# Optimization experiments

Measured on AMD Instinct MI355X. Metric: run time of the kernel, lower is better.

The kernel has to match this reference:

```python
import jax, jax.numpy as jnp
import numpy as np

DIM_Q = 1024
DIM_K = 1024
DIM_V = 1024


def setup_inputs() -> dict:
    key = jax.random.key(0)
    kx, kq, kk, kv = jax.random.split(key, 4)
    x = jax.random.normal(kx, (4, 2048, DIM_Q), dtype=jnp.float32)
    # torch nn.Linear weights: [out_features, in_features], y = x @ W.T
    scale = 1.0 / np.sqrt(DIM_Q)
    Wq = jax.random.uniform(kq, (DIM_K, DIM_Q), dtype=jnp.float32, minval=-scale, maxval=scale)
    Wk = jax.random.uniform(kk, (DIM_K, DIM_Q), dtype=jnp.float32, minval=-scale, maxval=scale)
    Wv = jax.random.uniform(kv, (DIM_V, DIM_Q), dtype=jnp.float32, minval=-scale, maxval=scale)
    return {"x": x, "Wq": Wq, "Wk": Wk, "Wv": Wv}


def reference(x, Wq, Wk, Wv):
    # q, k: [b, s, dim_k]; v: [b, s, dim_v]
    q = jnp.einsum('bsd,kd->bsk', x, Wq)
    k = jnp.einsum('bsd,kd->bsk', x, Wk)
    v = jnp.einsum('bsd,vd->bsv', x, Wv)
    norm_fact = 1.0 / jnp.sqrt(jnp.asarray(DIM_K, dtype=x.dtype))
    score = jnp.einsum('bik,bjk->bij', q, k) * norm_fact  # [b, s, s]
    score = jax.nn.softmax(score, axis=-1)
    att = jnp.einsum('bij,bjv->biv', score, v)
    att = att + v  # is_residual=True
    return att
```

## Files before the change

kernel.cpp:

```cpp
#include <hip/hip_runtime.h>
#include <hip/hip_bf16.h>

using bf16 = __hip_bfloat16;
typedef __attribute__((ext_vector_type(8))) short short8;
typedef __attribute__((ext_vector_type(4))) float floatx4;
typedef __attribute__((ext_vector_type(8))) int int8v;

__device__ __forceinline__ void async_ld16(const void* g, void* l) {
  __builtin_amdgcn_global_load_lds((const __attribute__((address_space(1))) void*)g,
                                   (__attribute__((address_space(3))) void*)l, 16, 0, 0);
}

__device__ __forceinline__ int pk4_fp8(float a, float b, float c, float d) {
  int v = __builtin_amdgcn_cvt_pk_fp8_f32(a, b, 0, false);
  return __builtin_amdgcn_cvt_pk_fp8_f32(c, d, v, true);
}


__device__ __forceinline__ void gemm_core(const bf16* __restrict__ At,
                                          const bf16* __restrict__ Bt,
                                          int K, bf16* lA, bf16* lB,
                                          floatx4 acc[4][4]) {
  const int tid  = threadIdx.x;
  const int w    = tid >> 6;
  const int lane = tid & 63;
  const int subM = (w >> 1) * 64;
  const int subN = (w & 1) * 64;
  const int fr   = lane & 15;
  const int fq   = lane >> 4;

  int srow[4], scol[4], sdst[4];
#pragma unroll
  for (int q = 0; q < 4; ++q) {
    int p = q * 256 + w * 64 + lane;
    int r = p >> 3;
    int j = (p & 7) ^ (r & 7);
    srow[q] = r;
    scol[q] = j * 8;
    sdst[q] = (q * 256 + w * 64) * 8;
  }
  int offA[2][4], offB[2][4];
#pragma unroll
  for (int kc = 0; kc < 2; ++kc)
#pragma unroll
    for (int i = 0; i < 4; ++i) {
      int rA = subM + i * 16 + fr;
      offA[kc][i] = (rA * 8 + ((kc * 4 + fq) ^ (rA & 7))) * 8;
      int rB = subN + i * 16 + fr;
      offB[kc][i] = (rB * 8 + ((kc * 4 + fq) ^ (rB & 7))) * 8;
    }

  floatx4 zero = {0.f, 0.f, 0.f, 0.f};
#pragma unroll
  for (int i = 0; i < 4; ++i)
#pragma unroll
    for (int j = 0; j < 4; ++j) acc[i][j] = zero;

  for (int k0 = 0; k0 < K; k0 += 64) {
    __syncthreads();
#pragma unroll
    for (int q = 0; q < 4; ++q) {
      async_ld16(At + (size_t)srow[q] * K + k0 + scol[q], lA + sdst[q]);
      async_ld16(Bt + (size_t)srow[q] * K + k0 + scol[q], lB + sdst[q]);
    }
    __syncthreads();
#pragma unroll
    for (int kc = 0; kc < 2; ++kc) {
      short8 a[4], b[4];
#pragma unroll
      for (int i = 0; i < 4; ++i) a[i] = *(const short8*)(lA + offA[kc][i]);
#pragma unroll
      for (int j = 0; j < 4; ++j) b[j] = *(const short8*)(lB + offB[kc][j]);
#pragma unroll
      for (int i = 0; i < 4; ++i)
#pragma unroll
        for (int j = 0; j < 4; ++j)
          acc[i][j] = __builtin_amdgcn_mfma_f32_16x16x32_bf16(a[i], b[j], acc[i][j], 0, 0, 0);
    }
  }
}

__device__ __forceinline__ void gemm_core_f8(const unsigned char* __restrict__ At,
                                             const unsigned char* __restrict__ Bt,
                                             int K, unsigned char* lA, unsigned char* lB,
                                             floatx4 acc[4][4]) {
  const int tid  = threadIdx.x;
  const int w    = tid >> 6;
  const int lane = tid & 63;
  const int subM = (w >> 1) * 64;
  const int subN = (w & 1) * 64;
  const int fr   = lane & 15;
  const int fq   = lane >> 4;

  int srow[4], scol[4], sdst[4];
#pragma unroll
  for (int q = 0; q < 4; ++q) {
    int p = q * 256 + w * 64 + lane;
    int r = p >> 3;
    int j = (p & 7) ^ (r & 7);
    srow[q] = r;
    scol[q] = j * 16;
    sdst[q] = (q * 256 + w * 64) * 16;
  }
  int offA[2][4], offB[2][4];
#pragma unroll
  for (int h = 0; h < 2; ++h)
#pragma unroll
    for (int i = 0; i < 4; ++i) {
      int rA = subM + i * 16 + fr;
      offA[h][i] = rA * 128 + (((fq * 2 + h) ^ (rA & 7)) * 16);
      int rB = subN + i * 16 + fr;
      offB[h][i] = rB * 128 + (((fq * 2 + h) ^ (rB & 7)) * 16);
    }

  floatx4 zero = {0.f, 0.f, 0.f, 0.f};
#pragma unroll
  for (int i = 0; i < 4; ++i)
#pragma unroll
    for (int j = 0; j < 4; ++j) acc[i][j] = zero;

  for (int k0 = 0; k0 < K; k0 += 128) {
    __syncthreads();
#pragma unroll
    for (int q = 0; q < 4; ++q) {
      async_ld16(At + (size_t)srow[q] * K + k0 + scol[q], lA + sdst[q]);
      async_ld16(Bt + (size_t)srow[q] * K + k0 + scol[q], lB + sdst[q]);
    }
    __syncthreads();
    int8v a[4], b[4];
#pragma unroll
    for (int i = 0; i < 4; ++i) {
      int4 lo = *(const int4*)(lA + offA[0][i]);
      int4 hi = *(const int4*)(lA + offA[1][i]);
      int8v v;
      v[0] = lo.x; v[1] = lo.y; v[2] = lo.z; v[3] = lo.w;
      v[4] = hi.x; v[5] = hi.y; v[6] = hi.z; v[7] = hi.w;
      a[i] = v;
    }
#pragma unroll
    for (int j = 0; j < 4; ++j) {
      int4 lo = *(const int4*)(lB + offB[0][j]);
      int4 hi = *(const int4*)(lB + offB[1][j]);
      int8v v;
      v[0] = lo.x; v[1] = lo.y; v[2] = lo.z; v[3] = lo.w;
      v[4] = hi.x; v[5] = hi.y; v[6] = hi.z; v[7] = hi.w;
      b[j] = v;
    }
#pragma unroll
    for (int i = 0; i < 4; ++i)
#pragma unroll
      for (int j = 0; j < 4; ++j)
        acc[i][j] = __builtin_amdgcn_mfma_scale_f32_16x16x128_f8f6f4(
            a[i], b[j], acc[i][j], 0, 0, 0, 0x7F7F7F7F, 0, 0x7F7F7F7F);
  }
}

__global__ __launch_bounds__(256) void proj_gemm(
    const bf16* __restrict__ Xbf, const bf16* __restrict__ Wvbf, bf16* __restrict__ Vbf,
    const unsigned char* __restrict__ X8, const unsigned char* __restrict__ Wq8,
    const unsigned char* __restrict__ Wk8,
    unsigned char* __restrict__ Qf8, unsigned char* __restrict__ Kf8) {
  __shared__ __align__(16) char lds[32768];
  const int id = blockIdx.x;
  const int tid = threadIdx.x, w = tid >> 6, lane = tid & 63;
  const int subM = (w >> 1) * 64, subN = (w & 1) * 64;
  const int fr = lane & 15, fq = lane >> 4;

  if (id < 512) {
    const int r = id & 7, g = id >> 3;
    const int ty = r * 8 + (g & 7), tx = g >> 3;
    bf16* lA = (bf16*)lds;
    bf16* lB = (bf16*)(lds + 16384);
    floatx4 acc[4][4];
    gemm_core(Xbf + (size_t)ty * 128 * 1024, Wvbf + (size_t)tx * 128 * 1024,
              1024, lA, lB, acc);
    const int rowBase = ty * 128 + subM;
    const int colBase = tx * 128 + subN;
#pragma unroll
    for (int i = 0; i < 4; ++i)
#pragma unroll
      for (int j = 0; j < 4; ++j)
#pragma unroll
        for (int rr = 0; rr < 4; ++rr) {
          int row = rowBase + i * 16 + fq * 4 + rr;
          int col = colBase + j * 16 + fr;
          Vbf[(size_t)row * 1024 + col] = __float2bfloat16(acc[i][j][rr]);
        }
  } else {
    const int local = id - 512;
    const int z = local >> 9, lid = local & 511;
    const int r = lid & 7, g = lid >> 3;
    const int ty = r * 8 + (g & 7), tx = g >> 3;
    unsigned char* lA = (unsigned char*)lds;
    unsigned char* lB = (unsigned char*)(lds + 16384);
    floatx4 acc[4][4];
    gemm_core_f8(X8 + (size_t)ty * 128 * 1024,
                 (z == 0 ? Wq8 : Wk8) + (size_t)tx * 128 * 1024, 1024, lA, lB, acc);
    unsigned char* dst = (z == 0) ? Qf8 : Kf8;
    const int rowBase = ty * 128 + subM;
    const int colBase = tx * 128 + subN;
#pragma unroll
    for (int i = 0; i < 4; ++i)
#pragma unroll
      for (int rr = 0; rr < 4; ++rr) {
        int row = rowBase + i * 16 + fq * 4 + rr;
        unsigned int p = (unsigned int)pk4_fp8(acc[i][0][rr], acc[i][1][rr],
                                               acc[i][2][rr], acc[i][3][rr]);
        *(unsigned int*)&dst[(size_t)row * 1024 + colBase + fr * 4] = p;
      }
  }
}

__global__ __launch_bounds__(256) void mid_kernel(
    const unsigned char* __restrict__ Qf8, const unsigned char* __restrict__ Kf8,
    unsigned char* __restrict__ S8, float* __restrict__ l,
    const bf16* __restrict__ Vbf, unsigned char* __restrict__ Vt8) {
  __shared__ __align__(16) char lds[32768];
  const int id = blockIdx.x;
  const int t = threadIdx.x;

  if (id < 1024) {
    const int r = id & 7, g = id >> 3;
    const int b = g >> 5;
    const int rem = g & 31;
    const int ty = r * 2 + (rem & 1);
    const int tx = rem >> 1;
    unsigned char* lA = (unsigned char*)lds;
    unsigned char* lB = (unsigned char*)(lds + 16384);
    floatx4 acc[4][4];
    gemm_core_f8(Qf8 + (size_t)b * 2048 * 1024 + (size_t)ty * 128 * 1024,
                 Kf8 + (size_t)b * 2048 * 1024 + (size_t)tx * 128 * 1024,
                 1024, lA, lB, acc);
    const int w = t >> 6, lane = t & 63;
    const int subM = (w >> 1) * 64, subN = (w & 1) * 64;
    const int fr = lane & 15, fq = lane >> 4;
    const int rowBase = ty * 128 + subM;
    const int colBase = tx * 128 + subN;
    unsigned char* Sb = S8 + (size_t)b * 2048 * 2048;
    float* lb = l + (size_t)b * 2048;
#pragma unroll
    for (int i = 0; i < 4; ++i)
#pragma unroll
      for (int rr = 0; rr < 4; ++rr) {
        int row = rowBase + i * 16 + fq * 4 + rr;
        unsigned int p = (unsigned int)pk4_fp8(
            __expf(acc[i][0][rr] * 0.03125f), __expf(acc[i][1][rr] * 0.03125f),
            __expf(acc[i][2][rr] * 0.03125f), __expf(acc[i][3][rr] * 0.03125f));
        *(unsigned int*)&Sb[(size_t)row * 2048 + colBase + fr * 4] = p;
        float psum = __builtin_amdgcn_cvt_f32_fp8(p, 0) + __builtin_amdgcn_cvt_f32_fp8(p, 1) +
                     __builtin_amdgcn_cvt_f32_fp8(p, 2) + __builtin_amdgcn_cvt_f32_fp8(p, 3);
        psum += __shfl_xor(psum, 1, 64);
        psum += __shfl_xor(psum, 2, 64);
        psum += __shfl_xor(psum, 4, 64);
        psum += __shfl_xor(psum, 8, 64);
        if (fr == 0) atomicAdd(&lb[row], psum);
      }
  } else {
    const int t2 = id - 1024;
    const int b = t2 >> 9, rem = t2 & 511;
    const int xs = rem & 31, yv = rem >> 5;
    const int s0 = xs * 64, v0 = yv * 64;
    short(*tile)[72] = (short(*)[72])lds;
#pragma unroll
    for (int i = 0; i < 2; ++i) {
      int c = t + i * 256;
      int row = c >> 3, cj = c & 7;
      *(short8*)&tile[row][cj * 8] =
          *(const short8*)&Vbf[((size_t)(b * 2048 + s0 + row)) * 1024 + v0 + cj * 8];
    }
    __syncthreads();
    const int vrow = t >> 2, sq = t & 3;
#pragma unroll
    for (int hc = 0; hc < 2; ++hc) {
      float f[8];
#pragma unroll
      for (int e = 0; e < 8; ++e) {
        int p = sq * 16 + hc * 8 + e;
        int s = (p & 3) * 16 + (p >> 2);
        short sh = tile[s][vrow];
        f[e] = __bfloat162float(*(bf16*)&sh);
      }
      uint2 packed;
      packed.x = (unsigned int)pk4_fp8(f[0], f[1], f[2], f[3]);
      packed.y = (unsigned int)pk4_fp8(f[4], f[5], f[6], f[7]);
      *(uint2*)&Vt8[((size_t)(b * 1024 + v0 + vrow)) * 2048 + s0 + sq * 16 + hc * 8] = packed;
    }
  }
}

__global__ __launch_bounds__(256) void pv_gemm(const unsigned char* __restrict__ S8,
                                               const unsigned char* __restrict__ Vt8,
                                               const bf16* __restrict__ Vbf,
                                               const float* __restrict__ l,
                                               float* __restrict__ out) {
  __shared__ __align__(16) char lds[32768];
  unsigned char* lA = (unsigned char*)lds;
  unsigned char* lB = (unsigned char*)(lds + 16384);
  const int id = blockIdx.x;
  const int r = id & 7, g = id >> 3;
  const int b = g >> 4;
  const int rem = g & 15;
  const int ty = r * 2 + (rem & 1);
  const int tx = rem >> 1;

  floatx4 acc[4][4];
  gemm_core_f8(S8 + (size_t)b * 2048 * 2048 + (size_t)ty * 128 * 2048,
               Vt8 + (size_t)b * 1024 * 2048 + (size_t)tx * 128 * 2048,
               2048, lA, lB, acc);

  const int tid = threadIdx.x, w = tid >> 6, lane = tid & 63;
  const int subM = (w >> 1) * 64, subN = (w & 1) * 64;
  const int fr = lane & 15, fq = lane >> 4;
  const int rowBase = ty * 128 + subM;
  const int colBase = tx * 128 + subN;
  const float* lb = l + (size_t)b * 2048;
#pragma unroll
  for (int i = 0; i < 4; ++i)
#pragma unroll
    for (int rr = 0; rr < 4; ++rr) {
      int row = rowBase + i * 16 + fq * 4 + rr;
      float inv = 1.0f / lb[row];
#pragma unroll
      for (int j = 0; j < 4; ++j) {
        int col = colBase + j * 16 + fr;
        size_t oi = ((size_t)b * 2048 + row) * 1024 + col;
        out[oi] = acc[i][j][rr] * inv + __bfloat162float(Vbf[oi]);
      }
    }
}

__global__ void cast_all(const float* __restrict__ x, const float* __restrict__ wq,
                         const float* __restrict__ wk, const float* __restrict__ wv,
                         bf16* __restrict__ Xbf, unsigned char* __restrict__ X8,
                         unsigned char* __restrict__ Wq8, unsigned char* __restrict__ Wk8,
                         bf16* __restrict__ Wvbf, float* __restrict__ l) {
  const int blk = blockIdx.x;
  const int t = threadIdx.x;
  if (blk < 8192) {
    int i = blk * 256 + t;
    float4 f = ((const float4*)x)[i];
    bf16 tmp[4] = {__float2bfloat16(f.x), __float2bfloat16(f.y),
                   __float2bfloat16(f.z), __float2bfloat16(f.w)};
    ((ushort4*)Xbf)[i] = *(const ushort4*)tmp;
    ((unsigned int*)X8)[i] = (unsigned int)pk4_fp8(f.x, f.y, f.z, f.w);
  } else if (blk < 10240) {
    const float* src = (blk < 9216) ? wq : wk;
    unsigned char* dst = (blk < 9216) ? Wq8 : Wk8;
    int i = ((blk - 8192) & 1023) * 256 + t;
    float4 f = ((const float4*)src)[i];
    ((unsigned int*)dst)[i] = (unsigned int)pk4_fp8(f.x, f.y, f.z, f.w);
  } else if (blk < 11264) {
    int i = (blk - 10240) * 256 + t;
    float4 f = ((const float4*)wv)[i];
    bf16 tmp[4] = {__float2bfloat16(f.x), __float2bfloat16(f.y),
                   __float2bfloat16(f.z), __float2bfloat16(f.w)};
    ((ushort4*)Wvbf)[i] = *(const ushort4*)tmp;
  } else {
    int i = (blk - 11264) * 256 + t;
    ((float4*)l)[i] = make_float4(0.f, 0.f, 0.f, 0.f);
  }
}

extern "C" void kernel_launch(void* const* d_in, const int* in_sizes, int n_in,
                              void* d_out, int out_size, void* d_ws, size_t ws_size,
                              hipStream_t stream) {
  const float* x  = (const float*)d_in[0];
  const float* Wq = (const float*)d_in[1];
  const float* Wk = (const float*)d_in[2];
  const float* Wv = (const float*)d_in[3];
  float* out = (float*)d_out;

  char* ws = (char*)d_ws;
  bf16* Xbf = (bf16*)ws;                   ws += (size_t)8192 * 1024 * 2;
  unsigned char* X8 = (unsigned char*)ws;  ws += (size_t)8192 * 1024;
  unsigned char* Wq8 = (unsigned char*)ws; ws += (size_t)1024 * 1024;
  unsigned char* Wk8 = (unsigned char*)ws; ws += (size_t)1024 * 1024;
  bf16* Wvbf = (bf16*)ws;                  ws += (size_t)1024 * 1024 * 2;
  unsigned char* Qf8 = (unsigned char*)ws; ws += (size_t)8192 * 1024;
  unsigned char* Kf8 = (unsigned char*)ws; ws += (size_t)8192 * 1024;
  bf16* Vbf = (bf16*)ws;                   ws += (size_t)8192 * 1024 * 2;
  unsigned char* Vt8 = (unsigned char*)ws; ws += (size_t)4 * 1024 * 2048;
  unsigned char* S8  = (unsigned char*)ws; ws += (size_t)4 * 2048 * 2048;
  float* l = (float*)ws;                   ws += (size_t)8192 * 4;

  cast_all<<<11272, 256, 0, stream>>>(x, Wq, Wk, Wv, Xbf, X8, Wq8, Wk8, Wvbf, l);
  proj_gemm<<<1536, 256, 0, stream>>>(Xbf, Wvbf, Vbf, X8, Wq8, Wk8, Qf8, Kf8);
  mid_kernel<<<3072, 256, 0, stream>>>(Qf8, Kf8, S8, l, Vbf, Vt8);
  pv_gemm<<<512, 256, 0, stream>>>(S8, Vt8, Vbf, l, out);
}
```

Baseline: 188.1 us.

## Widen FP8 GEMM tiles to 128x256 and extend LDS swizzle

Adds a 128x256 FP8 GEMM core used by the Q/K projection and the QK^T score kernel, which halves the block count and loads each A fragment once for eight MFMA columns instead of four. The LDS XOR swizzle gains an extra bit from row bit 3 to reduce bank conflicts on fragment reads. LDS grows to 48 KB and launch bounds request two blocks per CU. The wider accumulator raises register pressure, and fewer, larger blocks may leave some CUs underused.

```diff
diff --git a/kernel.cpp b/kernel.cpp
--- a/kernel.cpp
+++ b/kernel.cpp
@@ -14,6 +14,14 @@
 __device__ __forceinline__ int pk4_fp8(float a, float b, float c, float d) {
   int v = __builtin_amdgcn_cvt_pk_fp8_f32(a, b, 0, false);
   return __builtin_amdgcn_cvt_pk_fp8_f32(c, d, v, true);
+}
+
+__device__ __forceinline__ int8v ld_frag16(const unsigned char* lo, const unsigned char* hi) {
+  int4 l0 = *(const int4*)lo, h0 = *(const int4*)hi;
+  int8v v;
+  v[0] = l0.x; v[1] = l0.y; v[2] = l0.z; v[3] = l0.w;
+  v[4] = h0.x; v[5] = h0.y; v[6] = h0.z; v[7] = h0.w;
+  return v;
 }
 
 
@@ -97,7 +105,7 @@
   for (int q = 0; q < 4; ++q) {
     int p = q * 256 + w * 64 + lane;
     int r = p >> 3;
-    int j = (p & 7) ^ (r & 7);
+    int j = (p & 7) ^ (r & 7) ^ ((r & 8) >> 1);
     srow[q] = r;
     scol[q] = j * 16;
     sdst[q] = (q * 256 + w * 64) * 16;
@@ -108,9 +116,9 @@
 #pragma unroll
     for (int i = 0; i < 4; ++i) {
       int rA = subM + i * 16 + fr;
-      offA[h][i] = rA * 128 + (((fq * 2 + h) ^ (rA & 7)) * 16);
+      offA[h][i] = rA * 128 + (((fq * 2 + h) ^ (rA & 7) ^ ((rA & 8) >> 1)) * 16);
       int rB = subN + i * 16 + fr;
-      offB[h][i] = rB * 128 + (((fq * 2 + h) ^ (rB & 7)) * 16);
+      offB[h][i] = rB * 128 + (((fq * 2 + h) ^ (rB & 7) ^ ((rB & 8) >> 1)) * 16);
     }
 
   floatx4 zero = {0.f, 0.f, 0.f, 0.f};
@@ -129,23 +137,9 @@
     __syncthreads();
     int8v a[4], b[4];
 #pragma unroll
-    for (int i = 0; i < 4; ++i) {
-      int4 lo = *(const int4*)(lA + offA[0][i]);
-      int4 hi = *(const int4*)(lA + offA[1][i]);
-      int8v v;
-      v[0] = lo.x; v[1] = lo.y; v[2] = lo.z; v[3] = lo.w;
-      v[4] = hi.x; v[5] = hi.y; v[6] = hi.z; v[7] = hi.w;
-      a[i] = v;
-    }
-#pragma unroll
-    for (int j = 0; j < 4; ++j) {
-      int4 lo = *(const int4*)(lB + offB[0][j]);
-      int4 hi = *(const int4*)(lB + offB[1][j]);
-      int8v v;
-      v[0] = lo.x; v[1] = lo.y; v[2] = lo.z; v[3] = lo.w;
-      v[4] = hi.x; v[5] = hi.y; v[6] = hi.z; v[7] = hi.w;
-      b[j] = v;
-    }
+    for (int i = 0; i < 4; ++i) a[i] = ld_frag16(lA + offA[0][i], lA + offA[1][i]);
+#pragma unroll
+    for (int j = 0; j < 4; ++j) b[j] = ld_frag16(lB + offB[0][j], lB + offB[1][j]);
 #pragma unroll
     for (int i = 0; i < 4; ++i)
 #pragma unroll
@@ -155,15 +149,86 @@
   }
 }
 
-__global__ __launch_bounds__(256) void proj_gemm(
+__device__ __forceinline__ void gemm_core_f8_v2(const unsigned char* __restrict__ At,
+                                                const unsigned char* __restrict__ Bt,
+                                                int K, unsigned char* lA, unsigned char* lB,
+                                                floatx4 acc[4][8]) {
+  const int tid  = threadIdx.x;
+  const int w    = tid >> 6;
+  const int lane = tid & 63;
+  const int subM = (w >> 1) * 64;
+  const int subN = (w & 1) * 128;
+  const int fr   = lane & 15;
+  const int fq   = lane >> 4;
+
+  int srowA[4], scolA[4], sdstA[4];
+#pragma unroll
+  for (int q = 0; q < 4; ++q) {
+    int p = q * 256 + w * 64 + lane;
+    int r = p >> 3;
+    int j = (p & 7) ^ (r & 7) ^ ((r & 8) >> 1);
+    srowA[q] = r; scolA[q] = j * 16; sdstA[q] = (q * 256 + w * 64) * 16;
+  }
+  int srowB[8], scolB[8], sdstB[8];
+#pragma unroll
+  for (int q = 0; q < 8; ++q) {
+    int p = q * 256 + w * 64 + lane;
+    int r = p >> 3;
+    int j = (p & 7) ^ (r & 7) ^ ((r & 8) >> 1);
+    srowB[q] = r; scolB[q] = j * 16; sdstB[q] = (q * 256 + w * 64) * 16;
+  }
+  int offA[2][4], offB[2][8];
+#pragma unroll
+  for (int h = 0; h < 2; ++h) {
+#pragma unroll
+    for (int i = 0; i < 4; ++i) {
+      int rA = subM + i * 16 + fr;
+      offA[h][i] = rA * 128 + (((fq * 2 + h) ^ (rA & 7) ^ ((rA & 8) >> 1)) * 16);
+    }
+#pragma unroll
+    for (int j = 0; j < 8; ++j) {
+      int rB = subN + j * 16 + fr;
+      offB[h][j] = rB * 128 + (((fq * 2 + h) ^ (rB & 7) ^ ((rB & 8) >> 1)) * 16);
+    }
+  }
+
+  floatx4 zero = {0.f, 0.f, 0.f, 0.f};
+#pragma unroll
+  for (int i = 0; i < 4; ++i)
+#pragma unroll
+    for (int j = 0; j < 8; ++j) acc[i][j] = zero;
+
+  for (int k0 = 0; k0 < K; k0 += 128) {
+    __syncthreads();
+#pragma unroll
+    for (int q = 0; q < 4; ++q)
+      async_ld16(At + (size_t)srowA[q] * K + k0 + scolA[q], lA + sdstA[q]);
+#pragma unroll
+    for (int q = 0; q < 8; ++q)
+      async_ld16(Bt + (size_t)srowB[q] * K + k0 + scolB[q], lB + sdstB[q]);
+    __syncthreads();
+    int8v a[4];
+#pragma unroll
+    for (int i = 0; i < 4; ++i) a[i] = ld_frag16(lA + offA[0][i], lA + offA[1][i]);
+#pragma unroll
+    for (int j = 0; j < 8; ++j) {
+      int8v bf = ld_frag16(lB + offB[0][j], lB + offB[1][j]);
+#pragma unroll
+      for (int i = 0; i < 4; ++i)
+        acc[i][j] = __builtin_amdgcn_mfma_scale_f32_16x16x128_f8f6f4(
+            a[i], bf, acc[i][j], 0, 0, 0, 0x7F7F7F7F, 0, 0x7F7F7F7F);
+    }
+  }
+}
+
+__global__ __launch_bounds__(256, 2) void proj_gemm(
     const bf16* __restrict__ Xbf, const bf16* __restrict__ Wvbf, bf16* __restrict__ Vbf,
     const unsigned char* __restrict__ X8, const unsigned char* __restrict__ Wq8,
     const unsigned char* __restrict__ Wk8,
     unsigned char* __restrict__ Qf8, unsigned char* __restrict__ Kf8) {
-  __shared__ __align__(16) char lds[32768];
+  __shared__ __align__(16) char lds[49152];
   const int id = blockIdx.x;
   const int tid = threadIdx.x, w = tid >> 6, lane = tid & 63;
-  const int subM = (w >> 1) * 64, subN = (w & 1) * 64;
   const int fr = lane & 15, fq = lane >> 4;
 
   if (id < 512) {
@@ -174,6 +239,7 @@
     floatx4 acc[4][4];
     gemm_core(Xbf + (size_t)ty * 128 * 1024, Wvbf + (size_t)tx * 128 * 1024,
               1024, lA, lB, acc);
+    const int subM = (w >> 1) * 64, subN = (w & 1) * 64;
     const int rowBase = ty * 128 + subM;
     const int colBase = tx * 128 + subN;
 #pragma unroll
@@ -188,54 +254,59 @@
         }
   } else {
     const int local = id - 512;
-    const int z = local >> 9, lid = local & 511;
+    const int z = local >> 8, lid = local & 255;
     const int r = lid & 7, g = lid >> 3;
-    const int ty = r * 8 + (g & 7), tx = g >> 3;
+    const int ty = r * 8 + (g & 7);
+    const int tx = g >> 3;
     unsigned char* lA = (unsigned char*)lds;
     unsigned char* lB = (unsigned char*)(lds + 16384);
-    floatx4 acc[4][4];
-    gemm_core_f8(X8 + (size_t)ty * 128 * 1024,
-                 (z == 0 ? Wq8 : Wk8) + (size_t)tx * 128 * 1024, 1024, lA, lB, acc);
+    floatx4 acc[4][8];
+    gemm_core_f8_v2(X8 + (size_t)ty * 128 * 1024,
+                    (z == 0 ? Wq8 : Wk8) + (size_t)tx * 256 * 1024, 1024, lA, lB, acc);
     unsigned char* dst = (z == 0) ? Qf8 : Kf8;
+    const int subM = (w >> 1) * 64, subN = (w & 1) * 128;
     const int rowBase = ty * 128 + subM;
-    const int colBase = tx * 128 + subN;
+    const int colBase = tx * 256 + subN;
 #pragma unroll
     for (int i = 0; i < 4; ++i)
 #pragma unroll
       for (int rr = 0; rr < 4; ++rr) {
         int row = rowBase + i * 16 + fq * 4 + rr;
-        unsigned int p = (unsigned int)pk4_fp8(acc[i][0][rr], acc[i][1][rr],
-                                               acc[i][2][rr], acc[i][3][rr]);
-        *(unsigned int*)&dst[(size_t)row * 1024 + colBase + fr * 4] = p;
+        unsigned int p0 = (unsigned int)pk4_fp8(acc[i][0][rr], acc[i][1][rr],
+                                                acc[i][2][rr], acc[i][3][rr]);
+        unsigned int p1 = (unsigned int)pk4_fp8(acc[i][4][rr], acc[i][5][rr],
+                                                acc[i][6][rr], acc[i][7][rr]);
+        *(unsigned int*)&dst[(size_t)row * 1024 + colBase + fr * 4] = p0;
+        *(unsigned int*)&dst[(size_t)row * 1024 + colBase + 64 + fr * 4] = p1;
       }
   }
 }
 
-__global__ __launch_bounds__(256) void mid_kernel(
+__global__ __launch_bounds__(256, 2) void mid_kernel(
     const unsigned char* __restrict__ Qf8, const unsigned char* __restrict__ Kf8,
     unsigned char* __restrict__ S8, float* __restrict__ l,
     const bf16* __restrict__ Vbf, unsigned char* __restrict__ Vt8) {
-  __shared__ __align__(16) char lds[32768];
+  __shared__ __align__(16) char lds[49152];
   const int id = blockIdx.x;
   const int t = threadIdx.x;
 
-  if (id < 1024) {
+  if (id < 512) {
     const int r = id & 7, g = id >> 3;
-    const int b = g >> 5;
-    const int rem = g & 31;
+    const int b = g >> 4;
+    const int rem = g & 15;
     const int ty = r * 2 + (rem & 1);
     const int tx = rem >> 1;
     unsigned char* lA = (unsigned char*)lds;
     unsigned char* lB = (unsigned char*)(lds + 16384);
-    floatx4 acc[4][4];
-    gemm_core_f8(Qf8 + (size_t)b * 2048 * 1024 + (size_t)ty * 128 * 1024,
-                 Kf8 + (size_t)b * 2048 * 1024 + (size_t)tx * 128 * 1024,
-                 1024, lA, lB, acc);
+    floatx4 acc[4][8];
+    gemm_core_f8_v2(Qf8 + (size_t)b * 2048 * 1024 + (size_t)ty * 128 * 1024,
+                    Kf8 + (size_t)b * 2048 * 1024 + (size_t)tx * 256 * 1024,
+                    1024, lA, lB, acc);
     const int w = t >> 6, lane = t & 63;
-    const int subM = (w >> 1) * 64, subN = (w & 1) * 64;
+    const int subM = (w >> 1) * 64, subN = (w & 1) * 128;
     const int fr = lane & 15, fq = lane >> 4;
     const int rowBase = ty * 128 + subM;
-    const int colBase = tx * 128 + subN;
+    const int colBase = tx * 256 + subN;
     unsigned char* Sb = S8 + (size_t)b * 2048 * 2048;
     float* lb = l + (size_t)b * 2048;
 #pragma unroll
@@ -243,12 +314,18 @@
 #pragma unroll
       for (int rr = 0; rr < 4; ++rr) {
         int row = rowBase + i * 16 + fq * 4 + rr;
-        unsigned int p = (unsigned int)pk4_fp8(
+        unsigned int p0 = (unsigned int)pk4_fp8(
             __expf(acc[i][0][rr] * 0.03125f), __expf(acc[i][1][rr] * 0.03125f),
             __expf(acc[i][2][rr] * 0.03125f), __expf(acc[i][3][rr] * 0.03125f));
-        *(unsigned int*)&Sb[(size_t)row * 2048 + colBase + fr * 4] = p;
-        float psum = __builtin_amdgcn_cvt_f32_fp8(p, 0) + __builtin_amdgcn_cvt_f32_fp8(p, 1) +
-                     __builtin_amdgcn_cvt_f32_fp8(p, 2) + __builtin_amdgcn_cvt_f32_fp8(p, 3);
+        unsigned int p1 = (unsigned int)pk4_fp8(
+            __expf(acc[i][4][rr] * 0.03125f), __expf(acc[i][5][rr] * 0.03125f),
+            __expf(acc[i][6][rr] * 0.03125f), __expf(acc[i][7][rr] * 0.03125f));
+        *(unsigned int*)&Sb[(size_t)row * 2048 + colBase + fr * 4] = p0;
+        *(unsigned int*)&Sb[(size_t)row * 2048 + colBase + 64 + fr * 4] = p1;
+        float psum = __builtin_amdgcn_cvt_f32_fp8(p0, 0) + __builtin_amdgcn_cvt_f32_fp8(p0, 1) +
+                     __builtin_amdgcn_cvt_f32_fp8(p0, 2) + __builtin_amdgcn_cvt_f32_fp8(p0, 3) +
+                     __builtin_amdgcn_cvt_f32_fp8(p1, 0) + __builtin_amdgcn_cvt_f32_fp8(p1, 1) +
+                     __builtin_amdgcn_cvt_f32_fp8(p1, 2) + __builtin_amdgcn_cvt_f32_fp8(p1, 3);
         psum += __shfl_xor(psum, 1, 64);
         psum += __shfl_xor(psum, 2, 64);
         psum += __shfl_xor(psum, 4, 64);
@@ -256,7 +333,7 @@
         if (fr == 0) atomicAdd(&lb[row], psum);
       }
   } else {
-    const int t2 = id - 1024;
+    const int t2 = id - 512;
     const int b = t2 >> 9, rem = t2 & 511;
     const int xs = rem & 31, yv = rem >> 5;
     const int s0 = xs * 64, v0 = yv * 64;
@@ -384,7 +461,7 @@
   float* l = (float*)ws;                   ws += (size_t)8192 * 4;
 
   cast_all<<<11272, 256, 0, stream>>>(x, Wq, Wk, Wv, Xbf, X8, Wq8, Wk8, Wvbf, l);
-  proj_gemm<<<1536, 256, 0, stream>>>(Xbf, Wvbf, Vbf, X8, Wq8, Wk8, Qf8, Kf8);
-  mid_kernel<<<3072, 256, 0, stream>>>(Qf8, Kf8, S8, l, Vbf, Vt8);
+  proj_gemm<<<1024, 256, 0, stream>>>(Xbf, Wvbf, Vbf, X8, Wq8, Wk8, Qf8, Kf8);
+  mid_kernel<<<2560, 256, 0, stream>>>(Qf8, Kf8, S8, l, Vbf, Vt8);
   pv_gemm<<<512, 256, 0, stream>>>(S8, Vt8, Vbf, l, out);
 }
```

Result: faster. 176.3 us (-6.3%).
